# Kernel optimization log

Hardware: AMD Instinct MI355X
Metric: run time of the kernel (lower is better)

The kernel has to match this reference:

```python
import jax, jax.numpy as jnp
import numpy as np

N, T, D, H = 2, 2048, 1024, 16
DH = D // H  # per-head dim = 64


def setup_inputs() -> dict:
    key = jax.random.key(0)
    k1, k2, k3, k4 = jax.random.split(key, 4)
    x = jax.random.normal(k1, (N, T, D), dtype=jnp.float32)
    W = jax.random.normal(k2, (D, 3 * D), dtype=jnp.float32) * (D ** -0.5)
    proj_w = jax.random.normal(k3, (D, D), dtype=jnp.float32) * (D ** -0.5)
    proj_b = jax.random.normal(k4, (D,), dtype=jnp.float32) * 0.02
    return {"x": x, "W": W, "proj_w": proj_w, "proj_b": proj_b}


def reference(x, W, proj_w, proj_b):
    n, t, d = x.shape
    qkv = x @ W                                   # [N,T,3D]
    q, k, v = jnp.split(qkv, 3, axis=-1)          # each [N,T,D]
    def heads(a):
        return a.reshape(n, t, H, DH).transpose(0, 2, 1, 3)  # [N,H,T,DH]
    q, k, v = heads(q), heads(k), heads(v)
    scale = DH ** -0.5
    scores = jnp.einsum('nhtd,nhsd->nhts', q, k) * scale      # [N,H,T,T]
    causal = jnp.tril(jnp.ones((t, t), dtype=bool))
    scores = jnp.where(causal, scores, jnp.finfo(scores.dtype).min)
    w = jax.nn.softmax(scores, axis=-1)
    out = jnp.einsum('nhts,nhsd->nhtd', w, v)                 # [N,H,T,DH]
    out = out.transpose(0, 2, 1, 3).reshape(n, t, d)          # [N,T,D]
    return out @ proj_w.T + proj_b
```

## Files before the change

### kernel.cpp

```cpp
#include <hip/hip_runtime.h>
#include <hip/hip_bf16.h>
#include <stdint.h>

#define N_B 2
#define T_S 2048
#define D_M 1024
#define H_N 16
#define D_H 64

typedef __bf16 bf16_t;
typedef __bf16 bf16x8 __attribute__((ext_vector_type(8)));
typedef float f32x4 __attribute__((ext_vector_type(4)));

__device__ __forceinline__ void async_ld16(const void* g, void* lds_uniform_base) {
  __builtin_amdgcn_global_load_lds(
      (const __attribute__((address_space(1))) uint32_t*)(uintptr_t)g,
      (__attribute__((address_space(3))) uint32_t*)(uintptr_t)lds_uniform_base,
      16, 0, 0);
}

__global__ __launch_bounds__(256) void cvt_kernel(const float* __restrict__ in,
                                                  bf16_t* __restrict__ out, int n4) {
  int i = blockIdx.x * blockDim.x + threadIdx.x;
  if (i < n4) {
    float4 v = ((const float4*)in)[i];
    union { bf16_t b[4]; uint64_t u; } o;
    o.b[0] = (bf16_t)v.x; o.b[1] = (bf16_t)v.y;
    o.b[2] = (bf16_t)v.z; o.b[3] = (bf16_t)v.w;
    *(uint64_t*)(out + (size_t)i * 4) = o.u;
  }
}

__global__ __launch_bounds__(256) void transpose_cvt_kernel(const float* __restrict__ in,
                                                            bf16_t* __restrict__ out,
                                                            int R, int C) {
  __shared__ float tile[32][33];
  int bx = blockIdx.x * 32;
  int by = blockIdx.y * 32;
  int tx = threadIdx.x, ty = threadIdx.y;
#pragma unroll
  for (int i = 0; i < 32; i += 8)
    tile[ty + i][tx] = in[(size_t)(by + ty + i) * C + bx + tx];
  __syncthreads();
#pragma unroll
  for (int i = 0; i < 32; i += 8)
    out[(size_t)(bx + ty + i) * R + by + tx] = (bf16_t)tile[tx][ty + i];
}

template <int MODE>
__global__ __launch_bounds__(256) void gemm_bt_kernel(
    const bf16_t* __restrict__ A, const bf16_t* __restrict__ Bt,
    bf16_t* __restrict__ Qo, bf16_t* __restrict__ Ko, bf16_t* __restrict__ Vto,
    const float* __restrict__ bias, float* __restrict__ Co,
    int nbx, int cpx) {
  __shared__ bf16_t As[128 * 32];
  __shared__ bf16_t Bs[128 * 32];
  const int tid = threadIdx.x;
  const int lane = tid & 63;
  const int wid = tid >> 6;
  const int wr = wid >> 1, wc = wid & 1;
  const int g = lane >> 4, lr = lane & 15;
  const int d_ = blockIdx.x;
  const int orig = (d_ & 7) * cpx + (d_ >> 3);
  const int brow = (orig / nbx) * 128;
  const int bcol = (orig % nbx) * 128;

  f32x4 acc[4][4] = {};

  for (int k0 = 0; k0 < 1024; k0 += 32) {
#pragma unroll
    for (int q = 0; q < 2; ++q) {
      int idx = wid * 128 + q * 64 + lane;
      int row = idx >> 2, part = (idx & 3) * 8;
      async_ld16(A + (size_t)(brow + row) * 1024 + k0 + part,
                 &As[(wid * 128 + q * 64) * 8]);
      async_ld16(Bt + (size_t)(bcol + row) * 1024 + k0 + part,
                 &Bs[(wid * 128 + q * 64) * 8]);
    }
    __syncthreads();
    bf16x8 af[4], bfr[4];
#pragma unroll
    for (int i = 0; i < 4; ++i) {
      af[i]  = *(const bf16x8*)&As[(wr * 64 + i * 16 + lr) * 32 + g * 8];
      bfr[i] = *(const bf16x8*)&Bs[(wc * 64 + i * 16 + lr) * 32 + g * 8];
    }
#pragma unroll
    for (int i = 0; i < 4; ++i)
#pragma unroll
      for (int j = 0; j < 4; ++j)
        acc[i][j] = __builtin_amdgcn_mfma_f32_16x16x32_bf16(af[i], bfr[j], acc[i][j], 0, 0, 0);
    __syncthreads();
  }

#pragma unroll
  for (int i = 0; i < 4; ++i) {
    int row0 = brow + wr * 64 + i * 16 + g * 4;
#pragma unroll
    for (int j = 0; j < 4; ++j) {
      int col = bcol + wc * 64 + j * 16 + lr;
#pragma unroll
      for (int r = 0; r < 4; ++r) {
        int row = row0 + r;
        float v = acc[i][j][r];
        if (MODE == 0) {
          int n = row >> 11, t = row & (T_S - 1);
          int which = col >> 10, d = col & (D_M - 1);
          int h = d >> 6, dh = d & 63;
          if (which == 0)
            Qo[((size_t)(n * H_N + h) * T_S + t) * D_H + dh] = (bf16_t)v;
          else if (which == 1)
            Ko[((size_t)(n * H_N + h) * T_S + t) * D_H + dh] = (bf16_t)v;
          else
            Vto[((size_t)(n * H_N + h) * D_H + dh) * T_S + t] = (bf16_t)v;
        } else {
          Co[(size_t)row * D_M + col] = v + bias[col];
        }
      }
    }
  }
}

__global__ __launch_bounds__(256) void attn_kernel(const bf16_t* __restrict__ Q,
                                                   const bf16_t* __restrict__ K,
                                                   const bf16_t* __restrict__ Vt,
                                                   bf16_t* __restrict__ O) {
  __shared__ bf16_t Ks[3][4096];
  __shared__ bf16_t Vs[3][4096];
  __shared__ bf16_t Ps[4][1024];

  const int tid = threadIdx.x;
  const int lane = tid & 63;
  const int w = tid >> 6;
  const int g = lane >> 4, lr = lane & 15;
  const int d_ = blockIdx.x;
  const int orig = (d_ & 7) * 64 + (d_ >> 3);
  const int pair = orig & 15;
  const int nh = orig >> 4;
  const bf16_t* Qg = Q + (size_t)nh * T_S * D_H;
  const char* Kb = (const char*)(K + (size_t)nh * T_S * D_H);
  const char* Vb = (const char*)(Vt + (size_t)nh * D_H * T_S);
  const int n = nh >> 4, h = nh & 15;

  const int c0 = (w * 2 + 0) * 64 + lane;
  const int c1 = (w * 2 + 1) * 64 + lane;
  const int r0 = c0 >> 3, cb0 = (c0 & 7) * 16, sw0 = (r0 & 7) << 4;
  const int r1 = c1 >> 3, cb1 = (c1 & 7) * 16, sw1 = (r1 & 7) << 4;
  const int koff0 = r0 * 128 + (cb0 ^ sw0), koff1 = r1 * 128 + (cb1 ^ sw1);
  const int voff0 = r0 * 4096 + (cb0 ^ sw0), voff1 = r1 * 4096 + (cb1 ^ sw1);
  const int lds0 = (w * 2 + 0) * 1024, lds1 = (w * 2 + 1) * 1024;

  for (int half = 0; half < 2; ++half) {
    const int qc = half ? (31 - pair) : pair;
    const int q0 = qc * 64 + w * 16;
    const int nt = qc + 1;

    bf16x8 qf[2];
#pragma unroll
    for (int ks = 0; ks < 2; ++ks) {
      bf16x8 t = *(const bf16x8*)(Qg + (size_t)(q0 + lr) * D_H + ks * 32 + g * 8);
#pragma unroll
      for (int e = 0; e < 8; ++e) t[e] = (bf16_t)((float)t[e] * 0.125f);
      qf[ks] = t;
    }

    bf16x8 onesf;
#pragma unroll
    for (int e = 0; e < 8; ++e) onesf[e] = (bf16_t)1.0f;

    f32x4 o_acc[4] = {};
    f32x4 lacc = {};

    auto issue = [&](int t, int b) {
      const char* kt_ = Kb + (size_t)t * 8192;
      const char* vt_ = Vb + (size_t)t * 128;
      async_ld16(kt_ + koff0, (char*)Ks[b] + lds0);
      async_ld16(kt_ + koff1, (char*)Ks[b] + lds1);
      async_ld16(vt_ + voff0, (char*)Vs[b] + lds0);
      async_ld16(vt_ + voff1, (char*)Vs[b] + lds1);
    };

    auto compute = [&](int kt, int b, bool domask) {
      f32x4 s[4];
      __builtin_amdgcn_s_setprio(1);
#pragma unroll
      for (int j = 0; j < 4; ++j) {
        f32x4 a = {};
#pragma unroll
        for (int ks = 0; ks < 2; ++ks) {
          int row = j * 16 + lr;
          int cb = (ks * 32 + g * 8) * 2;
          bf16x8 kf = *(const bf16x8*)((char*)Ks[b] + ((row * 128 + cb) ^ ((row & 7) << 4)));
          a = __builtin_amdgcn_mfma_f32_16x16x32_bf16(qf[ks], kf, a, 0, 0, 0);
        }
        s[j] = a;
      }
      __builtin_amdgcn_s_setprio(0);

      if (domask) {
#pragma unroll
        for (int j = 0; j < 4; ++j)
#pragma unroll
          for (int r = 0; r < 4; ++r) {
            int kabs = kt * 64 + j * 16 + lr;
            int qabs = q0 + g * 4 + r;
            if (kabs > qabs) s[j][r] = -1.0e30f;
          }
      }

#pragma unroll
      for (int j = 0; j < 4; ++j)
#pragma unroll
        for (int r = 0; r < 4; ++r) {
          float sv = fminf(s[j][r] * 1.442695041f, 50.f);
          float p = __builtin_amdgcn_exp2f(sv);
          int row = g * 4 + r;
          int cb = (j * 16 + lr) * 2;
          *(bf16_t*)((char*)Ps[w] + ((row * 128 + cb) ^ ((row & 7) << 4))) = (bf16_t)p;
        }

      bf16x8 pf[2];
#pragma unroll
      for (int ks = 0; ks < 2; ++ks) {
        int cb = (ks * 32 + g * 8) * 2;
        pf[ks] = *(const bf16x8*)((char*)Ps[w] + ((lr * 128 + cb) ^ ((lr & 7) << 4)));
      }
      __builtin_amdgcn_s_setprio(1);
#pragma unroll
      for (int d = 0; d < 4; ++d) {
#pragma unroll
        for (int ks = 0; ks < 2; ++ks) {
          int row = d * 16 + lr;
          int cb = (ks * 32 + g * 8) * 2;
          bf16x8 vf = *(const bf16x8*)((char*)Vs[b] + ((row * 128 + cb) ^ ((row & 7) << 4)));
          o_acc[d] = __builtin_amdgcn_mfma_f32_16x16x32_bf16(pf[ks], vf, o_acc[d], 0, 0, 0);
        }
      }
#pragma unroll
      for (int ks = 0; ks < 2; ++ks)
        lacc = __builtin_amdgcn_mfma_f32_16x16x32_bf16(pf[ks], onesf, lacc, 0, 0, 0);
      __builtin_amdgcn_s_setprio(0);
    };

    issue(0, 0);
    if (nt > 1) issue(1, 1);

    for (int kt = 0; kt < nt - 1; ++kt) {
      asm volatile("s_waitcnt vmcnt(4)" ::: "memory");
      __builtin_amdgcn_s_barrier();
      __builtin_amdgcn_sched_barrier(0);
      if (kt + 2 < nt) issue(kt + 2, (kt + 2) % 3);
      compute(kt, kt % 3, false);
    }
    asm volatile("s_waitcnt vmcnt(0)" ::: "memory");
    __builtin_amdgcn_s_barrier();
    __builtin_amdgcn_sched_barrier(0);
    compute(nt - 1, (nt - 1) % 3, true);

#pragma unroll
    for (int r = 0; r < 4; ++r) {
      int t = q0 + g * 4 + r;
      float inv = 1.f / lacc[r];
#pragma unroll
      for (int d = 0; d < 4; ++d)
        O[(size_t)(n * T_S + t) * D_M + h * D_H + d * 16 + lr] = (bf16_t)(o_acc[d][r] * inv);
    }
    __syncthreads();
  }
}

extern "C" void kernel_launch(void* const* d_in, const int* in_sizes, int n_in,
                              void* d_out, int out_size, void* d_ws, size_t ws_size,
                              hipStream_t stream) {
  const float* x  = (const float*)d_in[0];
  const float* W  = (const float*)d_in[1];
  const float* pw = (const float*)d_in[2];
  const float* pb = (const float*)d_in[3];
  float* out = (float*)d_out;

  char* ws = (char*)d_ws;
  bf16_t* x_bf = (bf16_t*)(ws);
  bf16_t* Wt   = (bf16_t*)(ws + (8ull  << 20));
  bf16_t* pwb  = (bf16_t*)(ws + (14ull << 20));
  bf16_t* Qh   = (bf16_t*)(ws + (16ull << 20));
  bf16_t* Kh   = (bf16_t*)(ws + (24ull << 20));
  bf16_t* Vth  = (bf16_t*)(ws + (32ull << 20));
  bf16_t* Oa   = (bf16_t*)(ws + (40ull << 20));

  cvt_kernel<<<4096, 256, 0, stream>>>(x, x_bf, (4096 * 1024) / 4);
  transpose_cvt_kernel<<<dim3(96, 32), dim3(32, 8), 0, stream>>>(W, Wt, 1024, 3072);
  cvt_kernel<<<1024, 256, 0, stream>>>(pw, pwb, (1024 * 1024) / 4);

  gemm_bt_kernel<0><<<768, 256, 0, stream>>>(x_bf, Wt, Qh, Kh, Vth, nullptr, nullptr, 24, 96);

  attn_kernel<<<512, 256, 0, stream>>>(Qh, Kh, Vth, Oa);

  gemm_bt_kernel<1><<<256, 256, 0, stream>>>(Oa, pwb, nullptr, nullptr, nullptr, pb, out, 8, 32);
}
```

Baseline: 116.2 us.

## Use 2-wave attention blocks with 32 query rows per wave sharing K/V fragments

New measurement: 137.8 us. +18.5%, slower.

```diff
diff --git a/kernel.cpp b/kernel.cpp
--- a/kernel.cpp
+++ b/kernel.cpp
@@ -120,13 +120,13 @@
   }
 }
 
-__global__ __launch_bounds__(256) void attn_kernel(const bf16_t* __restrict__ Q,
+__global__ __launch_bounds__(128) void attn_kernel(const bf16_t* __restrict__ Q,
                                                    const bf16_t* __restrict__ K,
                                                    const bf16_t* __restrict__ Vt,
                                                    bf16_t* __restrict__ O) {
-  __shared__ bf16_t Ks[3][4096];
-  __shared__ bf16_t Vs[3][4096];
-  __shared__ bf16_t Ps[4][1024];
+  __shared__ bf16_t Ks[2][4096];
+  __shared__ bf16_t Vs[2][4096];
+  __shared__ bf16_t Ps[2][2048];
 
   const int tid = threadIdx.x;
   const int lane = tid & 63;
@@ -141,58 +141,65 @@
   const char* Vb = (const char*)(Vt + (size_t)nh * D_H * T_S);
   const int n = nh >> 4, h = nh & 15;
 
-  const int c0 = (w * 2 + 0) * 64 + lane;
-  const int c1 = (w * 2 + 1) * 64 + lane;
-  const int r0 = c0 >> 3, cb0 = (c0 & 7) * 16, sw0 = (r0 & 7) << 4;
-  const int r1 = c1 >> 3, cb1 = (c1 & 7) * 16, sw1 = (r1 & 7) << 4;
-  const int koff0 = r0 * 128 + (cb0 ^ sw0), koff1 = r1 * 128 + (cb1 ^ sw1);
-  const int voff0 = r0 * 4096 + (cb0 ^ sw0), voff1 = r1 * 4096 + (cb1 ^ sw1);
-  const int lds0 = (w * 2 + 0) * 1024, lds1 = (w * 2 + 1) * 1024;
+  int koff[4], voff[4];
+#pragma unroll
+  for (int q = 0; q < 4; ++q) {
+    int c = (w * 4 + q) * 64 + lane;
+    int r = c >> 3, cb = (c & 7) * 16, sw = (r & 7) << 4;
+    koff[q] = r * 128 + (cb ^ sw);
+    voff[q] = r * 4096 + (cb ^ sw);
+  }
 
   for (int half = 0; half < 2; ++half) {
     const int qc = half ? (31 - pair) : pair;
-    const int q0 = qc * 64 + w * 16;
+    const int q0 = qc * 64 + w * 32;
     const int nt = qc + 1;
 
-    bf16x8 qf[2];
+    bf16x8 qfA[2], qfB[2];
 #pragma unroll
     for (int ks = 0; ks < 2; ++ks) {
-      bf16x8 t = *(const bf16x8*)(Qg + (size_t)(q0 + lr) * D_H + ks * 32 + g * 8);
-#pragma unroll
-      for (int e = 0; e < 8; ++e) t[e] = (bf16_t)((float)t[e] * 0.125f);
-      qf[ks] = t;
+      bf16x8 ta = *(const bf16x8*)(Qg + (size_t)(q0 + lr) * D_H + ks * 32 + g * 8);
+      bf16x8 tb = *(const bf16x8*)(Qg + (size_t)(q0 + 16 + lr) * D_H + ks * 32 + g * 8);
+#pragma unroll
+      for (int e = 0; e < 8; ++e) {
+        ta[e] = (bf16_t)((float)ta[e] * 0.125f);
+        tb[e] = (bf16_t)((float)tb[e] * 0.125f);
+      }
+      qfA[ks] = ta; qfB[ks] = tb;
     }
 
     bf16x8 onesf;
 #pragma unroll
     for (int e = 0; e < 8; ++e) onesf[e] = (bf16_t)1.0f;
 
-    f32x4 o_acc[4] = {};
-    f32x4 lacc = {};
+    f32x4 oA[4] = {}, oB[4] = {};
+    f32x4 laccA = {}, laccB = {};
 
     auto issue = [&](int t, int b) {
       const char* kt_ = Kb + (size_t)t * 8192;
       const char* vt_ = Vb + (size_t)t * 128;
-      async_ld16(kt_ + koff0, (char*)Ks[b] + lds0);
-      async_ld16(kt_ + koff1, (char*)Ks[b] + lds1);
-      async_ld16(vt_ + voff0, (char*)Vs[b] + lds0);
-      async_ld16(vt_ + voff1, (char*)Vs[b] + lds1);
+#pragma unroll
+      for (int q = 0; q < 4; ++q) {
+        async_ld16(kt_ + koff[q], (char*)Ks[b] + (w * 4 + q) * 1024);
+        async_ld16(vt_ + voff[q], (char*)Vs[b] + (w * 4 + q) * 1024);
+      }
     };
 
     auto compute = [&](int kt, int b, bool domask) {
-      f32x4 s[4];
+      f32x4 sA[4], sB[4];
       __builtin_amdgcn_s_setprio(1);
 #pragma unroll
       for (int j = 0; j < 4; ++j) {
-        f32x4 a = {};
+        f32x4 a = {}, bb = {};
 #pragma unroll
         for (int ks = 0; ks < 2; ++ks) {
           int row = j * 16 + lr;
           int cb = (ks * 32 + g * 8) * 2;
           bf16x8 kf = *(const bf16x8*)((char*)Ks[b] + ((row * 128 + cb) ^ ((row & 7) << 4)));
-          a = __builtin_amdgcn_mfma_f32_16x16x32_bf16(qf[ks], kf, a, 0, 0, 0);
+          a  = __builtin_amdgcn_mfma_f32_16x16x32_bf16(qfA[ks], kf, a, 0, 0, 0);
+          bb = __builtin_amdgcn_mfma_f32_16x16x32_bf16(qfB[ks], kf, bb, 0, 0, 0);
         }
-        s[j] = a;
+        sA[j] = a; sB[j] = bb;
       }
       __builtin_amdgcn_s_setprio(0);
 
@@ -202,8 +209,9 @@
 #pragma unroll
           for (int r = 0; r < 4; ++r) {
             int kabs = kt * 64 + j * 16 + lr;
-            int qabs = q0 + g * 4 + r;
-            if (kabs > qabs) s[j][r] = -1.0e30f;
+            int qa = q0 + g * 4 + r;
+            if (kabs > qa) sA[j][r] = -1.0e30f;
+            if (kabs > qa + 16) sB[j][r] = -1.0e30f;
           }
       }
 
@@ -211,18 +219,26 @@
       for (int j = 0; j < 4; ++j)
 #pragma unroll
         for (int r = 0; r < 4; ++r) {
-          float sv = fminf(s[j][r] * 1.442695041f, 50.f);
-          float p = __builtin_amdgcn_exp2f(sv);
-          int row = g * 4 + r;
           int cb = (j * 16 + lr) * 2;
-          *(bf16_t*)((char*)Ps[w] + ((row * 128 + cb) ^ ((row & 7) << 4))) = (bf16_t)p;
+          {
+            float p = __builtin_amdgcn_exp2f(fminf(sA[j][r] * 1.442695041f, 50.f));
+            int row = g * 4 + r;
+            *(bf16_t*)((char*)Ps[w] + ((row * 128 + cb) ^ ((row & 7) << 4))) = (bf16_t)p;
+          }
+          {
+            float p = __builtin_amdgcn_exp2f(fminf(sB[j][r] * 1.442695041f, 50.f));
+            int row = 16 + g * 4 + r;
+            *(bf16_t*)((char*)Ps[w] + ((row * 128 + cb) ^ ((row & 7) << 4))) = (bf16_t)p;
+          }
         }
 
-      bf16x8 pf[2];
+      bf16x8 pA[2], pB[2];
 #pragma unroll
       for (int ks = 0; ks < 2; ++ks) {
         int cb = (ks * 32 + g * 8) * 2;
-        pf[ks] = *(const bf16x8*)((char*)Ps[w] + ((lr * 128 + cb) ^ ((lr & 7) << 4)));
+        int ra = lr, rb = 16 + lr;
+        pA[ks] = *(const bf16x8*)((char*)Ps[w] + ((ra * 128 + cb) ^ ((ra & 7) << 4)));
+        pB[ks] = *(const bf16x8*)((char*)Ps[w] + ((rb * 128 + cb) ^ ((rb & 7) << 4)));
       }
       __builtin_amdgcn_s_setprio(1);
 #pragma unroll
@@ -232,37 +248,39 @@
           int row = d * 16 + lr;
           int cb = (ks * 32 + g * 8) * 2;
           bf16x8 vf = *(const bf16x8*)((char*)Vs[b] + ((row * 128 + cb) ^ ((row & 7) << 4)));
-          o_acc[d] = __builtin_amdgcn_mfma_f32_16x16x32_bf16(pf[ks], vf, o_acc[d], 0, 0, 0);
+          oA[d] = __builtin_amdgcn_mfma_f32_16x16x32_bf16(pA[ks], vf, oA[d], 0, 0, 0);
+          oB[d] = __builtin_amdgcn_mfma_f32_16x16x32_bf16(pB[ks], vf, oB[d], 0, 0, 0);
         }
       }
 #pragma unroll
-      for (int ks = 0; ks < 2; ++ks)
-        lacc = __builtin_amdgcn_mfma_f32_16x16x32_bf16(pf[ks], onesf, lacc, 0, 0, 0);
+      for (int ks = 0; ks < 2; ++ks) {
+        laccA = __builtin_amdgcn_mfma_f32_16x16x32_bf16(pA[ks], onesf, laccA, 0, 0, 0);
+        laccB = __builtin_amdgcn_mfma_f32_16x16x32_bf16(pB[ks], onesf, laccB, 0, 0, 0);
+      }
       __builtin_amdgcn_s_setprio(0);
     };
 
     issue(0, 0);
-    if (nt > 1) issue(1, 1);
-
-    for (int kt = 0; kt < nt - 1; ++kt) {
-      asm volatile("s_waitcnt vmcnt(4)" ::: "memory");
+    int buf = 0;
+    for (int kt = 0; kt < nt; ++kt) {
+      asm volatile("s_waitcnt vmcnt(0)" ::: "memory");
       __builtin_amdgcn_s_barrier();
       __builtin_amdgcn_sched_barrier(0);
-      if (kt + 2 < nt) issue(kt + 2, (kt + 2) % 3);
-      compute(kt, kt % 3, false);
-    }
-    asm volatile("s_waitcnt vmcnt(0)" ::: "memory");
-    __builtin_amdgcn_s_barrier();
-    __builtin_amdgcn_sched_barrier(0);
-    compute(nt - 1, (nt - 1) % 3, true);
+      if (kt + 1 < nt) issue(kt + 1, buf ^ 1);
+      compute(kt, buf, kt == nt - 1);
+      buf ^= 1;
+    }
 
 #pragma unroll
     for (int r = 0; r < 4; ++r) {
-      int t = q0 + g * 4 + r;
-      float inv = 1.f / lacc[r];
-#pragma unroll
-      for (int d = 0; d < 4; ++d)
-        O[(size_t)(n * T_S + t) * D_M + h * D_H + d * 16 + lr] = (bf16_t)(o_acc[d][r] * inv);
+      int ta = q0 + g * 4 + r;
+      float invA = 1.f / laccA[r];
+      float invB = 1.f / laccB[r];
+#pragma unroll
+      for (int d = 0; d < 4; ++d) {
+        O[(size_t)(n * T_S + ta) * D_M + h * D_H + d * 16 + lr] = (bf16_t)(oA[d][r] * invA);
+        O[(size_t)(n * T_S + ta + 16) * D_M + h * D_H + d * 16 + lr] = (bf16_t)(oB[d][r] * invB);
+      }
     }
     __syncthreads();
   }
@@ -292,7 +310,7 @@
 
   gemm_bt_kernel<0><<<768, 256, 0, stream>>>(x_bf, Wt, Qh, Kh, Vth, nullptr, nullptr, 24, 96);
 
-  attn_kernel<<<512, 256, 0, stream>>>(Qh, Kh, Vth, Oa);
+  attn_kernel<<<512, 128, 0, stream>>>(Qh, Kh, Vth, Oa);
 
   gemm_bt_kernel<1><<<256, 256, 0, stream>>>(Oa, pwb, nullptr, nullptr, nullptr, pb, out, 8, 32);
 }
```

## Split attention into one block per query chunk with heavy-first ordering

Applied to the files above, without the earlier changes.

New measurement: 116.1 us. No clear change (-0.1%).

```diff
diff --git a/kernel.cpp b/kernel.cpp
--- a/kernel.cpp
+++ b/kernel.cpp
@@ -124,18 +124,23 @@
                                                    const bf16_t* __restrict__ K,
                                                    const bf16_t* __restrict__ Vt,
                                                    bf16_t* __restrict__ O) {
-  __shared__ bf16_t Ks[3][4096];
-  __shared__ bf16_t Vs[3][4096];
+  __shared__ bf16_t Ks[2][4096];
+  __shared__ bf16_t Vs[2][4096];
   __shared__ bf16_t Ps[4][1024];
 
   const int tid = threadIdx.x;
   const int lane = tid & 63;
   const int w = tid >> 6;
   const int g = lane >> 4, lr = lane & 15;
+
   const int d_ = blockIdx.x;
-  const int orig = (d_ & 7) * 64 + (d_ >> 3);
-  const int pair = orig & 15;
-  const int nh = orig >> 4;
+  const int x = d_ & 7;
+  const int s = d_ >> 3;
+  const int hs = s & 3, j_ = s >> 2;
+  const int t_ = j_ >> 3, m_ = j_ & 7;
+  const int qc = (t_ == 0) ? (31 - m_) : (t_ == 1) ? (16 + m_)
+               : (t_ == 2) ? (15 - m_) : m_;
+  const int nh = x * 4 + hs;
   const bf16_t* Qg = Q + (size_t)nh * T_S * D_H;
   const char* Kb = (const char*)(K + (size_t)nh * T_S * D_H);
   const char* Vb = (const char*)(Vt + (size_t)nh * D_H * T_S);
@@ -149,122 +154,114 @@
   const int voff0 = r0 * 4096 + (cb0 ^ sw0), voff1 = r1 * 4096 + (cb1 ^ sw1);
   const int lds0 = (w * 2 + 0) * 1024, lds1 = (w * 2 + 1) * 1024;
 
-  for (int half = 0; half < 2; ++half) {
-    const int qc = half ? (31 - pair) : pair;
-    const int q0 = qc * 64 + w * 16;
-    const int nt = qc + 1;
-
-    bf16x8 qf[2];
+  const int q0 = qc * 64 + w * 16;
+  const int nt = qc + 1;
+
+  bf16x8 qf[2];
+#pragma unroll
+  for (int ks = 0; ks < 2; ++ks) {
+    bf16x8 t = *(const bf16x8*)(Qg + (size_t)(q0 + lr) * D_H + ks * 32 + g * 8);
+#pragma unroll
+    for (int e = 0; e < 8; ++e) t[e] = (bf16_t)((float)t[e] * 0.125f);
+    qf[ks] = t;
+  }
+
+  bf16x8 onesf;
+#pragma unroll
+  for (int e = 0; e < 8; ++e) onesf[e] = (bf16_t)1.0f;
+
+  f32x4 o_acc[4] = {};
+  f32x4 lacc = {};
+
+  auto issue = [&](int t, int b) {
+    const char* kt_ = Kb + (size_t)t * 8192;
+    const char* vt_ = Vb + (size_t)t * 128;
+    async_ld16(kt_ + koff0, (char*)Ks[b] + lds0);
+    async_ld16(kt_ + koff1, (char*)Ks[b] + lds1);
+    async_ld16(vt_ + voff0, (char*)Vs[b] + lds0);
+    async_ld16(vt_ + voff1, (char*)Vs[b] + lds1);
+  };
+
+  auto compute = [&](int kt, int b, bool domask) {
+    f32x4 s_[4];
+    __builtin_amdgcn_s_setprio(1);
+#pragma unroll
+    for (int j = 0; j < 4; ++j) {
+      f32x4 a = {};
+#pragma unroll
+      for (int ks = 0; ks < 2; ++ks) {
+        int row = j * 16 + lr;
+        int cb = (ks * 32 + g * 8) * 2;
+        bf16x8 kf = *(const bf16x8*)((char*)Ks[b] + ((row * 128 + cb) ^ ((row & 7) << 4)));
+        a = __builtin_amdgcn_mfma_f32_16x16x32_bf16(qf[ks], kf, a, 0, 0, 0);
+      }
+      s_[j] = a;
+    }
+    __builtin_amdgcn_s_setprio(0);
+
+    if (domask) {
+#pragma unroll
+      for (int j = 0; j < 4; ++j)
+#pragma unroll
+        for (int r = 0; r < 4; ++r) {
+          int kabs = kt * 64 + j * 16 + lr;
+          int qabs = q0 + g * 4 + r;
+          if (kabs > qabs) s_[j][r] = -1.0e30f;
+        }
+    }
+
+#pragma unroll
+    for (int j = 0; j < 4; ++j)
+#pragma unroll
+      for (int r = 0; r < 4; ++r) {
+        float sv = fminf(s_[j][r] * 1.442695041f, 50.f);
+        float p = __builtin_amdgcn_exp2f(sv);
+        int row = g * 4 + r;
+        int cb = (j * 16 + lr) * 2;
+        *(bf16_t*)((char*)Ps[w] + ((row * 128 + cb) ^ ((row & 7) << 4))) = (bf16_t)p;
+      }
+
+    bf16x8 pf[2];
 #pragma unroll
     for (int ks = 0; ks < 2; ++ks) {
-      bf16x8 t = *(const bf16x8*)(Qg + (size_t)(q0 + lr) * D_H + ks * 32 + g * 8);
-#pragma unroll
-      for (int e = 0; e < 8; ++e) t[e] = (bf16_t)((float)t[e] * 0.125f);
-      qf[ks] = t;
-    }
-
-    bf16x8 onesf;
-#pragma unroll
-    for (int e = 0; e < 8; ++e) onesf[e] = (bf16_t)1.0f;
-
-    f32x4 o_acc[4] = {};
-    f32x4 lacc = {};
-
-    auto issue = [&](int t, int b) {
-      const char* kt_ = Kb + (size_t)t * 8192;
-      const char* vt_ = Vb + (size_t)t * 128;
-      async_ld16(kt_ + koff0, (char*)Ks[b] + lds0);
-      async_ld16(kt_ + koff1, (char*)Ks[b] + lds1);
-      async_ld16(vt_ + voff0, (char*)Vs[b] + lds0);
-      async_ld16(vt_ + voff1, (char*)Vs[b] + lds1);
-    };
-
-    auto compute = [&](int kt, int b, bool domask) {
-      f32x4 s[4];
-      __builtin_amdgcn_s_setprio(1);
-#pragma unroll
-      for (int j = 0; j < 4; ++j) {
-        f32x4 a = {};
-#pragma unroll
-        for (int ks = 0; ks < 2; ++ks) {
-          int row = j * 16 + lr;
-          int cb = (ks * 32 + g * 8) * 2;
-          bf16x8 kf = *(const bf16x8*)((char*)Ks[b] + ((row * 128 + cb) ^ ((row & 7) << 4)));
-          a = __builtin_amdgcn_mfma_f32_16x16x32_bf16(qf[ks], kf, a, 0, 0, 0);
-        }
-        s[j] = a;
-      }
-      __builtin_amdgcn_s_setprio(0);
-
-      if (domask) {
-#pragma unroll
-        for (int j = 0; j < 4; ++j)
-#pragma unroll
-          for (int r = 0; r < 4; ++r) {
-            int kabs = kt * 64 + j * 16 + lr;
-            int qabs = q0 + g * 4 + r;
-            if (kabs > qabs) s[j][r] = -1.0e30f;
-          }
-      }
-
-#pragma unroll
-      for (int j = 0; j < 4; ++j)
-#pragma unroll
-        for (int r = 0; r < 4; ++r) {
-          float sv = fminf(s[j][r] * 1.442695041f, 50.f);
-          float p = __builtin_amdgcn_exp2f(sv);
-          int row = g * 4 + r;
-          int cb = (j * 16 + lr) * 2;
-          *(bf16_t*)((char*)Ps[w] + ((row * 128 + cb) ^ ((row & 7) << 4))) = (bf16_t)p;
-        }
-
-      bf16x8 pf[2];
+      int cb = (ks * 32 + g * 8) * 2;
+      pf[ks] = *(const bf16x8*)((char*)Ps[w] + ((lr * 128 + cb) ^ ((lr & 7) << 4)));
+    }
+    __builtin_amdgcn_s_setprio(1);
+#pragma unroll
+    for (int d = 0; d < 4; ++d) {
 #pragma unroll
       for (int ks = 0; ks < 2; ++ks) {
+        int row = d * 16 + lr;
         int cb = (ks * 32 + g * 8) * 2;
-        pf[ks] = *(const bf16x8*)((char*)Ps[w] + ((lr * 128 + cb) ^ ((lr & 7) << 4)));
-      }
-      __builtin_amdgcn_s_setprio(1);
-#pragma unroll
-      for (int d = 0; d < 4; ++d) {
-#pragma unroll
-        for (int ks = 0; ks < 2; ++ks) {
-          int row = d * 16 + lr;
-          int cb = (ks * 32 + g * 8) * 2;
-          bf16x8 vf = *(const bf16x8*)((char*)Vs[b] + ((row * 128 + cb) ^ ((row & 7) << 4)));
-          o_acc[d] = __builtin_amdgcn_mfma_f32_16x16x32_bf16(pf[ks], vf, o_acc[d], 0, 0, 0);
-        }
-      }
-#pragma unroll
-      for (int ks = 0; ks < 2; ++ks)
-        lacc = __builtin_amdgcn_mfma_f32_16x16x32_bf16(pf[ks], onesf, lacc, 0, 0, 0);
-      __builtin_amdgcn_s_setprio(0);
-    };
-
-    issue(0, 0);
-    if (nt > 1) issue(1, 1);
-
-    for (int kt = 0; kt < nt - 1; ++kt) {
-      asm volatile("s_waitcnt vmcnt(4)" ::: "memory");
-      __builtin_amdgcn_s_barrier();
-      __builtin_amdgcn_sched_barrier(0);
-      if (kt + 2 < nt) issue(kt + 2, (kt + 2) % 3);
-      compute(kt, kt % 3, false);
-    }
+        bf16x8 vf = *(const bf16x8*)((char*)Vs[b] + ((row * 128 + cb) ^ ((row & 7) << 4)));
+        o_acc[d] = __builtin_amdgcn_mfma_f32_16x16x32_bf16(pf[ks], vf, o_acc[d], 0, 0, 0);
+      }
+    }
+#pragma unroll
+    for (int ks = 0; ks < 2; ++ks)
+      lacc = __builtin_amdgcn_mfma_f32_16x16x32_bf16(pf[ks], onesf, lacc, 0, 0, 0);
+    __builtin_amdgcn_s_setprio(0);
+  };
+
+  issue(0, 0);
+  int buf = 0;
+  for (int kt = 0; kt < nt; ++kt) {
     asm volatile("s_waitcnt vmcnt(0)" ::: "memory");
     __builtin_amdgcn_s_barrier();
     __builtin_amdgcn_sched_barrier(0);
-    compute(nt - 1, (nt - 1) % 3, true);
-
-#pragma unroll
-    for (int r = 0; r < 4; ++r) {
-      int t = q0 + g * 4 + r;
-      float inv = 1.f / lacc[r];
-#pragma unroll
-      for (int d = 0; d < 4; ++d)
-        O[(size_t)(n * T_S + t) * D_M + h * D_H + d * 16 + lr] = (bf16_t)(o_acc[d][r] * inv);
-    }
-    __syncthreads();
+    if (kt + 1 < nt) issue(kt + 1, buf ^ 1);
+    compute(kt, buf, kt == nt - 1);
+    buf ^= 1;
+  }
+
+#pragma unroll
+  for (int r = 0; r < 4; ++r) {
+    int t = q0 + g * 4 + r;
+    float inv = 1.f / lacc[r];
+#pragma unroll
+    for (int d = 0; d < 4; ++d)
+      O[(size_t)(n * T_S + t) * D_M + h * D_H + d * 16 + lr] = (bf16_t)(o_acc[d][r] * inv);
   }
 }
 
@@ -292,7 +289,7 @@
 
   gemm_bt_kernel<0><<<768, 256, 0, stream>>>(x_bf, Wt, Qh, Kh, Vth, nullptr, nullptr, 24, 96);
 
-  attn_kernel<<<512, 256, 0, stream>>>(Qh, Kh, Vth, Oa);
+  attn_kernel<<<1024, 256, 0, stream>>>(Qh, Kh, Vth, Oa);
 
   gemm_bt_kernel<1><<<256, 256, 0, stream>>>(Oa, pwb, nullptr, nullptr, nullptr, pb, out, 8, 32);
 }
```
